# Optimization experiments

Measured on AMD Instinct MI355X. Metric: run time of the kernel, lower is better.

Reference implementation:

```python
import jax, jax.numpy as jnp
import numpy as np

D_MODEL = 1024
BATCH, SEQ = 4, 4096


def setup_inputs() -> dict:
    key = jax.random.key(0)
    ks = jax.random.split(key, 4)
    scale = 1.0 / np.sqrt(D_MODEL)  # lecun_normal-ish init for Dense kernels
    x = jax.random.normal(ks[0], (BATCH, SEQ, D_MODEL), dtype=jnp.float32)
    Wf = jax.random.normal(ks[1], (D_MODEL, D_MODEL), dtype=jnp.float32) * scale
    Wi = jax.random.normal(ks[2], (D_MODEL, D_MODEL), dtype=jnp.float32) * scale
    Wb = jax.random.normal(ks[3], (D_MODEL, D_MODEL), dtype=jnp.float32) * scale
    bf = jnp.full((D_MODEL,), -4.0, dtype=jnp.float32)  # forget bias -> f~0.018
    bi = jnp.full((D_MODEL,), 4.0, dtype=jnp.float32)   # input bias  -> i~0.982
    bb = jnp.zeros((D_MODEL,), dtype=jnp.float32)
    return {"x": x, "Wf": Wf, "bf": bf, "Wi": Wi, "bi": bi, "Wb": Wb, "bb": bb}


def _scan_combine(c1, c2):
    a1, b1 = c1
    a2, b2 = c2
    # linear recurrence composition: h = a2*(a1*h_prev + b1) + b2
    return a1 * a2, a2 * b1 + b2


def reference(x, Wf, bf, Wi, bi, Wb, bb):
    # gates + drive: [B, S, D]
    f = jax.nn.sigmoid(jnp.einsum('bsd,de->bse', x, Wf) + bf)
    i = jax.nn.sigmoid(jnp.einsum('bsd,de->bse', x, Wi) + bi)
    b = (jnp.einsum('bsd,de->bse', x, Wb) + bb) / jnp.sqrt(jnp.float32(x.shape[-1]))
    a = (1.0 - f).astype(jnp.complex64)
    b_gated = (i * b).astype(jnp.complex64)
    # parallel associative scan over time axis: h_t = a_t * h_{t-1} + b_t
    _, state = jax.lax.associative_scan(_scan_combine, (a, b_gated), axis=1)
    return state.real
```

## Files before the change

kernel.cpp:

```cpp
#include <hip/hip_runtime.h>
#include <cstdint>

#define D_MODEL 1024
#define BATCH 4
#define SEQ 4096
#define M_TOT (BATCH*SEQ)

#define BM 128
#define BNG 64
#define BK 64
#define NKT (D_MODEL/BK)

#define XS_BYTES (BM*BK*2)
#define WG_BYTES (BNG*BK*2)
#define TILE_BYTES (XS_BYTES + 3*WG_BYTES)
#define SMEM_BYTES (2*TILE_BYTES)

#define NCHUNK 64
#define CHUNK 64

typedef __bf16 bf16x8 __attribute__((ext_vector_type(8)));
typedef float f32x4 __attribute__((ext_vector_type(4)));
typedef unsigned short u16x8 __attribute__((ext_vector_type(8)));

static __device__ __forceinline__ unsigned short f2bf(float f) {
    unsigned int u = __float_as_uint(f);
    return (unsigned short)((u + 0x7fffu + ((u >> 16) & 1u)) >> 16);
}
static __device__ __forceinline__ float ubf(unsigned short u) {
    return __uint_as_float((unsigned int)u << 16);
}

__global__ void k_convert_x(const float* __restrict__ x, unsigned short* __restrict__ xb) {
    int i = blockIdx.x * 256 + threadIdx.x;
    const float4* p = (const float4*)x;
    float4 v0 = p[2*i], v1 = p[2*i+1];
    u16x8 r;
    r[0] = f2bf(v0.x); r[1] = f2bf(v0.y); r[2] = f2bf(v0.z); r[3] = f2bf(v0.w);
    r[4] = f2bf(v1.x); r[5] = f2bf(v1.y); r[6] = f2bf(v1.z); r[7] = f2bf(v1.w);
    *(u16x8*)(xb + (size_t)i * 8) = r;
}

__global__ void k_transpose_w(const float* __restrict__ Wf, const float* __restrict__ Wi,
                              const float* __restrict__ Wb, unsigned short* __restrict__ wt) {
    __shared__ float tile[32][33];
    int g = blockIdx.z;
    const float* W = (g == 0) ? Wf : (g == 1) ? Wi : Wb;
    int n0 = blockIdx.x * 32, k0 = blockIdx.y * 32;
    int tx = threadIdx.x, ty = threadIdx.y;
    for (int j = 0; j < 4; ++j)
        tile[ty + j*8][tx] = W[(size_t)(k0 + ty + j*8) * D_MODEL + n0 + tx];
    __syncthreads();
    for (int j = 0; j < 4; ++j) {
        int n = n0 + ty + j*8;
        wt[(size_t)g * D_MODEL * D_MODEL + (size_t)n * D_MODEL + k0 + tx] = f2bf(tile[tx][ty + j*8]);
    }
}

#define GL16(gp, lp) \
    __builtin_amdgcn_global_load_lds((const __attribute__((address_space(1))) void*)(gp), \
                                     (__attribute__((address_space(3))) void*)(lp), 16, 0, 0)

__launch_bounds__(256, 2)
__global__ void k_gemm_gates(const unsigned short* __restrict__ xb, const unsigned short* __restrict__ wt,
                             const float* __restrict__ bfv, const float* __restrict__ biv,
                             const float* __restrict__ bbv,
                             unsigned int* __restrict__ fbg_out,
                             float* __restrict__ Ac, float* __restrict__ Bc) {
    extern __shared__ char smem[];
    const int tid  = threadIdx.x;
    const int wave = tid >> 6;
    const int lane = tid & 63;
    const int lr = lane & 15, lg = lane >> 4;
    const int bid = blockIdx.x;
    const int swz = (bid & 7) * 256 + (bid >> 3);
    const int mb = swz >> 4;
    const int nb = swz & 15;
    const int m0 = mb * BM;
    const int n0 = nb * BNG;
    const int wr = wave >> 1;
    const int wc = wave & 1;
    const int wrow = wr * 64;
    const int wcol = wc * 32;

    const int srl = tid >> 3;
    const int scb = ((tid & 7) * 16) ^ ((srl & 7) << 4);
    const unsigned short* sA  = xb + (size_t)(m0 + srl) * D_MODEL + (scb >> 1);
    const unsigned short* sB0 = wt + 0ull*D_MODEL*D_MODEL + (size_t)(n0 + srl) * D_MODEL + (scb >> 1);
    const unsigned short* sB1 = wt + 1ull*D_MODEL*D_MODEL + (size_t)(n0 + srl) * D_MODEL + (scb >> 1);
    const unsigned short* sB2 = wt + 2ull*D_MODEL*D_MODEL + (size_t)(n0 + srl) * D_MODEL + (scb >> 1);

#define STAGE(db) do { \
        char* _d = smem + (db)*TILE_BYTES + wave*1024; \
        GL16(sA + 0*32*D_MODEL, _d + 0*4096); \
        GL16(sA + 1*32*D_MODEL, _d + 1*4096); \
        GL16(sA + 2*32*D_MODEL, _d + 2*4096); \
        GL16(sA + 3*32*D_MODEL, _d + 3*4096); \
        char* _e = _d + XS_BYTES; \
        GL16(sB0,                _e + 0*4096); \
        GL16(sB0 + 32*D_MODEL,   _e + 1*4096); \
        GL16(sB1,                _e + 2*4096); \
        GL16(sB1 + 32*D_MODEL,   _e + 3*4096); \
        GL16(sB2,                _e + 4*4096); \
        GL16(sB2 + 32*D_MODEL,   _e + 5*4096); \
        sA += BK; sB0 += BK; sB1 += BK; sB2 += BK; \
    } while (0)

    f32x4 acc[3][4][2] = {};
    const int sxor = (lr & 7) << 4;

    STAGE(0);
    __syncthreads();

    for (int kt = 0; kt < NKT; ++kt) {
        if (kt + 1 < NKT) STAGE((kt + 1) & 1);
        const char* tb = smem + (kt & 1) * TILE_BYTES;
        #pragma unroll
        for (int kk = 0; kk < 2; ++kk) {
            const int ko = (kk*64 + lg*16) ^ sxor;
            bf16x8 bw[3][2];
            #pragma unroll
            for (int g = 0; g < 3; ++g)
                #pragma unroll
                for (int ni = 0; ni < 2; ++ni)
                    bw[g][ni] = *(const bf16x8*)(tb + XS_BYTES + g*WG_BYTES +
                                                 (wcol + ni*16 + lr)*128 + ko);
            bf16x8 af[4];
            #pragma unroll
            for (int mi = 0; mi < 4; ++mi)
                af[mi] = *(const bf16x8*)(tb + (wrow + mi*16 + lr)*128 + ko);
            #pragma unroll
            for (int g = 0; g < 3; ++g)
                #pragma unroll
                for (int mi = 0; mi < 4; ++mi)
                    #pragma unroll
                    for (int ni = 0; ni < 2; ++ni)
                        acc[g][mi][ni] = __builtin_amdgcn_mfma_f32_16x16x32_bf16(
                            af[mi], bw[g][ni], acc[g][mi][ni], 0, 0, 0);
        }
        __syncthreads();
    }

    #pragma unroll
    for (int ni = 0; ni < 2; ++ni) {
        const int col = n0 + wcol + ni*16 + lr;
        const float vbf = bfv[col], vbi = biv[col], vbb = bbv[col];
        float qA[4], qB[4];
        #pragma unroll
        for (int mi = 0; mi < 4; ++mi) {
            float Ap = 1.0f, Bp = 0.0f;
            #pragma unroll
            for (int r = 0; r < 4; ++r) {
                const int row = m0 + wrow + mi*16 + lg*4 + r;
                const float zf = acc[0][mi][ni][r] + vbf;
                const float zi = acc[1][mi][ni][r] + vbi;
                const float zb = (acc[2][mi][ni][r] + vbb) * 0.03125f;
                const float fg = 1.0f / (1.0f + __expf(-zf));
                const float ig = 1.0f / (1.0f + __expf(-zi));
                const unsigned short fu  = f2bf(fg);
                const unsigned short bgu = f2bf(ig * zb);
                const float a_r  = 1.0f - ubf(fu);
                const float bg_r = ubf(bgu);
                fbg_out[(size_t)row * D_MODEL + col] =
                    (unsigned int)fu | ((unsigned int)bgu << 16);
                Bp = fmaf(a_r, Bp, bg_r);
                Ap *= a_r;
            }
            qA[mi] = Ap; qB[mi] = Bp;
        }
        float CA = 1.0f, CB = 0.0f;
        #pragma unroll
        for (int q = 0; q < 4; ++q) {
            float A = qA[q], B = qB[q];
            float Ao = __shfl_xor(A, 16), Bo = __shfl_xor(B, 16);
            float B1 = (lg & 1) ? fmaf(A, Bo, B) : fmaf(Ao, B, Bo);
            float A1 = A * Ao;
            Ao = __shfl_xor(A1, 32); Bo = __shfl_xor(B1, 32);
            float B2 = (lg & 2) ? fmaf(A1, Bo, B1) : fmaf(Ao, B1, Bo);
            float A2 = A1 * Ao;
            CB = fmaf(A2, CB, B2);
            CA = CA * A2;
        }
        if (lg == 0) {
            const int chG = mb * 2 + wr;
            Ac[(size_t)chG * D_MODEL + col] = CA;
            Bc[(size_t)chG * D_MODEL + col] = CB;
        }
    }
#undef STAGE
}

__global__ void k_chunk_prefix(const float* __restrict__ Ac, const float* __restrict__ Bc,
                               float* __restrict__ H) {
    const int d = (blockIdx.x & 3) * 256 + threadIdx.x;
    const int b = blockIdx.x >> 2;
    float h = 0.0f;
    for (int c = 0; c < NCHUNK; ++c) {
        const size_t o = ((size_t)b * NCHUNK + c) * D_MODEL + d;
        H[o] = h;
        h = fmaf(Ac[o], h, Bc[o]);
    }
}

__global__ void k_apply(const unsigned int* __restrict__ fbg,
                        const float* __restrict__ H, float* __restrict__ out) {
    const int d0 = (blockIdx.x & 1) * 512 + threadIdx.x * 2;
    const int c = (blockIdx.x >> 1) & 63;
    const int b = blockIdx.x >> 7;
    const size_t base = ((size_t)b * SEQ + (size_t)c * CHUNK) * D_MODEL + d0;
    const size_t hoff = ((size_t)b * NCHUNK + c) * D_MODEL + d0;
    float h0 = H[hoff], h1 = H[hoff + 1];
    for (int t = 0; t < CHUNK; ++t) {
        const size_t o = base + (size_t)t * D_MODEL;
        const uint2 v = *(const uint2*)(fbg + o);
        const float a0 = 1.0f - __uint_as_float(v.x << 16);
        const float b0 = __uint_as_float(v.x & 0xffff0000u);
        const float a1 = 1.0f - __uint_as_float(v.y << 16);
        const float b1 = __uint_as_float(v.y & 0xffff0000u);
        h0 = fmaf(a0, h0, b0);
        h1 = fmaf(a1, h1, b1);
        *(float2*)(out + o) = make_float2(h0, h1);
    }
}

extern "C" void kernel_launch(void* const* d_in, const int* in_sizes, int n_in,
                              void* d_out, int out_size, void* d_ws, size_t ws_size,
                              hipStream_t stream) {
    const float* x   = (const float*)d_in[0];
    const float* Wf  = (const float*)d_in[1];
    const float* bfv = (const float*)d_in[2];
    const float* Wi  = (const float*)d_in[3];
    const float* biv = (const float*)d_in[4];
    const float* Wb  = (const float*)d_in[5];
    const float* bbv = (const float*)d_in[6];
    float* out = (float*)d_out;

    char* ws = (char*)d_ws;
    unsigned int*   fbg   = (unsigned int*)ws;
    unsigned short* xb    = (unsigned short*)(ws + (64ull << 20));
    unsigned short* wt    = (unsigned short*)(ws + (96ull << 20));
    float* Ac = (float*)(ws + (102ull << 20));
    float* Bc = (float*)(ws + (103ull << 20));
    float* Hb = (float*)(ws + (64ull << 20));

    hipFuncSetAttribute((const void*)k_gemm_gates,
                        hipFuncAttributeMaxDynamicSharedMemorySize, SMEM_BYTES);

    hipLaunchKernelGGL(k_convert_x, dim3((M_TOT * D_MODEL / 8) / 256), dim3(256), 0, stream, x, xb);
    hipLaunchKernelGGL(k_transpose_w, dim3(32, 32, 3), dim3(32, 8), 0, stream, Wf, Wi, Wb, wt);
    hipLaunchKernelGGL(k_gemm_gates, dim3((M_TOT / BM) * (D_MODEL / BNG)), dim3(256), SMEM_BYTES, stream,
                       xb, wt, bfv, biv, bbv, fbg, Ac, Bc);
    hipLaunchKernelGGL(k_chunk_prefix, dim3(BATCH * (D_MODEL / 256)), dim3(256), 0, stream,
                       Ac, Bc, Hb);
    hipLaunchKernelGGL(k_apply, dim3(BATCH * NCHUNK * 2), dim3(256), 0, stream,
                       fbg, Hb, out);
}
```

Measured before the change: 167.5 us.

## Double GEMM block to eight waves with narrower per-wave output tiles

The gated GEMM kernel moves from 256 to 512 threads per block. Each wave now computes a 64x16 output slice for the three gates instead of 64x32, and each thread issues fewer global-to-LDS staging loads. The aim is more waves in flight to hide memory and MFMA latency. In exchange, each B fragment is reused across fewer MFMAs. The tighter launch bound (512 threads, 4 blocks) also caps the register budget, which risks spills, and LDS capacity may keep that occupancy target from being reached.

```diff
diff --git a/kernel.cpp b/kernel.cpp
--- a/kernel.cpp
+++ b/kernel.cpp
@@ -61,7 +61,7 @@
     __builtin_amdgcn_global_load_lds((const __attribute__((address_space(1))) void*)(gp), \
                                      (__attribute__((address_space(3))) void*)(lp), 16, 0, 0)
 
-__launch_bounds__(256, 2)
+__launch_bounds__(512, 4)
 __global__ void k_gemm_gates(const unsigned short* __restrict__ xb, const unsigned short* __restrict__ wt,
                              const float* __restrict__ bfv, const float* __restrict__ biv,
                              const float* __restrict__ bbv,
@@ -78,35 +78,30 @@
     const int nb = swz & 15;
     const int m0 = mb * BM;
     const int n0 = nb * BNG;
-    const int wr = wave >> 1;
-    const int wc = wave & 1;
+    const int wr = wave >> 2;
+    const int wc = wave & 3;
     const int wrow = wr * 64;
-    const int wcol = wc * 32;
-
-    const int srl = tid >> 3;
-    const int scb = ((tid & 7) * 16) ^ ((srl & 7) << 4);
-    const unsigned short* sA  = xb + (size_t)(m0 + srl) * D_MODEL + (scb >> 1);
-    const unsigned short* sB0 = wt + 0ull*D_MODEL*D_MODEL + (size_t)(n0 + srl) * D_MODEL + (scb >> 1);
-    const unsigned short* sB1 = wt + 1ull*D_MODEL*D_MODEL + (size_t)(n0 + srl) * D_MODEL + (scb >> 1);
-    const unsigned short* sB2 = wt + 2ull*D_MODEL*D_MODEL + (size_t)(n0 + srl) * D_MODEL + (scb >> 1);
+    const int wcol = wc * 16;
+
+    const int srow = tid >> 3;
+    const int scb  = ((tid & 7) * 16) ^ ((srow & 7) << 4);
+    const unsigned short* sA  = xb + (size_t)(m0 + srow) * D_MODEL + (scb >> 1);
+    const unsigned short* sB0 = wt + 0ull*D_MODEL*D_MODEL + (size_t)(n0 + srow) * D_MODEL + (scb >> 1);
+    const unsigned short* sB1 = wt + 1ull*D_MODEL*D_MODEL + (size_t)(n0 + srow) * D_MODEL + (scb >> 1);
+    const unsigned short* sB2 = wt + 2ull*D_MODEL*D_MODEL + (size_t)(n0 + srow) * D_MODEL + (scb >> 1);
 
 #define STAGE(db) do { \
         char* _d = smem + (db)*TILE_BYTES + wave*1024; \
-        GL16(sA + 0*32*D_MODEL, _d + 0*4096); \
-        GL16(sA + 1*32*D_MODEL, _d + 1*4096); \
-        GL16(sA + 2*32*D_MODEL, _d + 2*4096); \
-        GL16(sA + 3*32*D_MODEL, _d + 3*4096); \
+        GL16(sA,               _d + 0*8192); \
+        GL16(sA + 64*D_MODEL,  _d + 1*8192); \
         char* _e = _d + XS_BYTES; \
-        GL16(sB0,                _e + 0*4096); \
-        GL16(sB0 + 32*D_MODEL,   _e + 1*4096); \
-        GL16(sB1,                _e + 2*4096); \
-        GL16(sB1 + 32*D_MODEL,   _e + 3*4096); \
-        GL16(sB2,                _e + 4*4096); \
-        GL16(sB2 + 32*D_MODEL,   _e + 5*4096); \
+        GL16(sB0, _e + 0*8192); \
+        GL16(sB1, _e + 1*8192); \
+        GL16(sB2, _e + 2*8192); \
         sA += BK; sB0 += BK; sB1 += BK; sB2 += BK; \
     } while (0)
 
-    f32x4 acc[3][4][2] = {};
+    f32x4 acc[3][4] = {};
     const int sxor = (lr & 7) << 4;
 
     STAGE(0);
@@ -118,32 +113,26 @@
         #pragma unroll
         for (int kk = 0; kk < 2; ++kk) {
             const int ko = (kk*64 + lg*16) ^ sxor;
-            bf16x8 bw[3][2];
-            #pragma unroll
-            for (int g = 0; g < 3; ++g)
-                #pragma unroll
-                for (int ni = 0; ni < 2; ++ni)
-                    bw[g][ni] = *(const bf16x8*)(tb + XS_BYTES + g*WG_BYTES +
-                                                 (wcol + ni*16 + lr)*128 + ko);
+            const int bro = (wcol + lr)*128 + ko;
+            bf16x8 bw0 = *(const bf16x8*)(tb + XS_BYTES + 0*WG_BYTES + bro);
+            bf16x8 bw1 = *(const bf16x8*)(tb + XS_BYTES + 1*WG_BYTES + bro);
+            bf16x8 bw2 = *(const bf16x8*)(tb + XS_BYTES + 2*WG_BYTES + bro);
             bf16x8 af[4];
             #pragma unroll
             for (int mi = 0; mi < 4; ++mi)
                 af[mi] = *(const bf16x8*)(tb + (wrow + mi*16 + lr)*128 + ko);
             #pragma unroll
-            for (int g = 0; g < 3; ++g)
-                #pragma unroll
-                for (int mi = 0; mi < 4; ++mi)
-                    #pragma unroll
-                    for (int ni = 0; ni < 2; ++ni)
-                        acc[g][mi][ni] = __builtin_amdgcn_mfma_f32_16x16x32_bf16(
-                            af[mi], bw[g][ni], acc[g][mi][ni], 0, 0, 0);
+            for (int mi = 0; mi < 4; ++mi) {
+                acc[0][mi] = __builtin_amdgcn_mfma_f32_16x16x32_bf16(af[mi], bw0, acc[0][mi], 0,0,0);
+                acc[1][mi] = __builtin_amdgcn_mfma_f32_16x16x32_bf16(af[mi], bw1, acc[1][mi], 0,0,0);
+                acc[2][mi] = __builtin_amdgcn_mfma_f32_16x16x32_bf16(af[mi], bw2, acc[2][mi], 0,0,0);
+            }
         }
         __syncthreads();
     }
 
-    #pragma unroll
-    for (int ni = 0; ni < 2; ++ni) {
-        const int col = n0 + wcol + ni*16 + lr;
+    {
+        const int col = n0 + wcol + lr;
         const float vbf = bfv[col], vbi = biv[col], vbb = bbv[col];
         float qA[4], qB[4];
         #pragma unroll
@@ -152,9 +141,9 @@
             #pragma unroll
             for (int r = 0; r < 4; ++r) {
                 const int row = m0 + wrow + mi*16 + lg*4 + r;
-                const float zf = acc[0][mi][ni][r] + vbf;
-                const float zi = acc[1][mi][ni][r] + vbi;
-                const float zb = (acc[2][mi][ni][r] + vbb) * 0.03125f;
+                const float zf = acc[0][mi][r] + vbf;
+                const float zi = acc[1][mi][r] + vbi;
+                const float zb = (acc[2][mi][r] + vbb) * 0.03125f;
                 const float fg = 1.0f / (1.0f + __expf(-zf));
                 const float ig = 1.0f / (1.0f + __expf(-zi));
                 const unsigned short fu  = f2bf(fg);
@@ -248,7 +237,7 @@
 
     hipLaunchKernelGGL(k_convert_x, dim3((M_TOT * D_MODEL / 8) / 256), dim3(256), 0, stream, x, xb);
     hipLaunchKernelGGL(k_transpose_w, dim3(32, 32, 3), dim3(32, 8), 0, stream, Wf, Wi, Wb, wt);
-    hipLaunchKernelGGL(k_gemm_gates, dim3((M_TOT / BM) * (D_MODEL / BNG)), dim3(256), SMEM_BYTES, stream,
+    hipLaunchKernelGGL(k_gemm_gates, dim3((M_TOT / BM) * (D_MODEL / BNG)), dim3(512), SMEM_BYTES, stream,
                        xb, wt, bfv, biv, bbv, fbg, Ac, Bc);
     hipLaunchKernelGGL(k_chunk_prefix, dim3(BATCH * (D_MODEL / 256)), dim3(256), 0, stream,
                        Ac, Bc, Hb);
```

Result: faster. 160.2 us (-4.4%).
